# Optimization experiments

Hardware: AMD Instinct MI355X
Metric: run time of the kernel (lower is better)

Reference implementation:

```python
import jax, jax.numpy as jnp
import numpy as np

WS = 8          # window_size
SHIFT = 4       # shift_size
HEADS = 8
HD = 32         # head_dim
DIM = 256       # embedding_dim
PWS = 8         # pretrained_window_size
EPS = 1e-5


def _rel_tables():
    # log-spaced relative coords table, shape ((2*WS-1)^2, 2)
    r = np.arange(-(WS - 1), WS, dtype=np.float32)
    tb = np.stack(np.meshgrid(r, r, indexing='ij'), 0).reshape(2, -1).T
    tb = tb / (PWS - 1) * 8.0
    tb = np.sign(tb) * np.log2(np.abs(tb) + 1.0) / np.log2(8.0)
    # relative position index, shape (m, m)
    ch = np.arange(WS)
    coords = np.stack(np.meshgrid(ch, ch, indexing='ij'), 0).reshape(2, -1)
    rel = (coords[:, :, None] - coords[:, None, :]).transpose(1, 2, 0).astype(np.int64)
    rel[..., 0] += WS - 1
    rel[..., 1] += WS - 1
    rel[..., 0] *= 2 * WS - 1
    return tb.astype(np.float32), rel.sum(-1)


def _shift_mask(h, w):
    # standard Swin SW-MSA mask: region labels -> -100 where regions differ
    img = np.zeros((h, w), np.int32)
    cnt = 0
    for hs in (slice(0, h - WS), slice(h - WS, h - SHIFT), slice(h - SHIFT, h)):
        for wsl in (slice(0, w - WS), slice(w - WS, w - SHIFT), slice(w - SHIFT, w)):
            img[hs, wsl] = cnt
            cnt += 1
    nh, nw = h // WS, w // WS
    m = WS * WS
    mw = img.reshape(nh, WS, nw, WS).transpose(0, 2, 1, 3).reshape(nh * nw, m)
    return np.where(mw[:, None, :] != mw[:, :, None], -100.0, 0.0).astype(np.float32)


def _ln(x, g, b):
    mu = x.mean(-1, keepdims=True)
    var = ((x - mu) ** 2).mean(-1, keepdims=True)
    return (x - mu) * jax.lax.rsqrt(var + EPS) * g + b


def setup_inputs() -> dict:
    key = jax.random.key(0)
    ks = jax.random.split(key, 8)
    s = 0.02
    return {
        'x': jax.random.normal(ks[0], (2, DIM, 256, 256), jnp.float32),
        'qkv_w': jax.random.normal(ks[1], (DIM, 3 * HEADS * HD), jnp.float32) * s,
        'logit_scale': jnp.full((HEADS,), np.log(10.0), jnp.float32),
        'proj_w': jax.random.normal(ks[2], (HEADS * HD, DIM), jnp.float32) * s,
        'proj_b': jnp.zeros((DIM,), jnp.float32),
        'ln1_w': jnp.ones((DIM,), jnp.float32),
        'ln1_b': jnp.zeros((DIM,), jnp.float32),
        'fc1_w': jax.random.normal(ks[3], (DIM, 4 * DIM), jnp.float32) * s,
        'fc1_b': jnp.zeros((4 * DIM,), jnp.float32),
        'fc2_w': jax.random.normal(ks[4], (4 * DIM, DIM), jnp.float32) * s,
        'fc2_b': jnp.zeros((DIM,), jnp.float32),
        'ln2_w': jnp.ones((DIM,), jnp.float32),
        'ln2_b': jnp.zeros((DIM,), jnp.float32),
        'cpb_w1': jax.random.normal(ks[5], (2, 512), jnp.float32) * s,
        'cpb_b1': jnp.zeros((512,), jnp.float32),
        'cpb_w2': jax.random.normal(ks[6], (512, HEADS), jnp.float32) * s,
    }


def reference(x, qkv_w, logit_scale, proj_w, proj_b, ln1_w, ln1_b,
              fc1_w, fc1_b, fc2_w, fc2_b, ln2_w, ln2_b,
              cpb_w1, cpb_b1, cpb_w2):
    b, c, h, w = x.shape
    nh, nw = h // WS, w // WS
    Nw, m = nh * nw, WS * WS
    tb_np, idx_np = _rel_tables()
    smask = jnp.asarray(_shift_mask(h, w))              # (Nw, m, m)

    # cyclic shift
    xs = jnp.roll(x, (-SHIFT, -SHIFT), axis=(2, 3))

    # relative position bias via MLP, then 16*sigmoid
    bt = jax.nn.relu(jnp.asarray(tb_np) @ cpb_w1 + cpb_b1) @ cpb_w2   # (T, H)
    rpe = bt[jnp.asarray(idx_np).reshape(-1)].reshape(m, m, HEADS)
    bias = 16.0 * jax.nn.sigmoid(rpe.transpose(2, 0, 1))              # (H, m, m)
    amask = bias[None] + smask[:, None]                               # (Nw, H, m, m)

    # window partition: (b, c, h, w) -> (b, Nw, m, c)
    xw = xs.reshape(b, c, nh, WS, nw, WS).transpose(0, 2, 4, 3, 5, 1).reshape(b, Nw, m, c)

    # cosine attention
    qkv = (xw @ qkv_w).reshape(b, Nw, m, 3, HEADS, HD).transpose(3, 0, 1, 4, 2, 5)
    q, k, v = qkv[0], qkv[1], qkv[2]                                  # (b, Nw, H, m, HD)
    qn = q / jnp.maximum(jnp.linalg.norm(q, axis=-1, keepdims=True), 1e-12)
    kn = k / jnp.maximum(jnp.linalg.norm(k, axis=-1, keepdims=True), 1e-12)
    scale = jnp.exp(jnp.minimum(logit_scale, np.log(100.0)))          # (H,)
    logits = jnp.einsum('bnhid,bnhjd->bnhij', qn, kn) * scale[None, None, :, None, None]
    logits = logits + amask[None]
    p = jax.nn.softmax(logits, axis=-1)
    o = jnp.einsum('bnhij,bnhjd->bnhid', p, v)
    o = o.transpose(0, 1, 3, 2, 4).reshape(b, Nw, m, HEADS * HD) @ proj_w + proj_b

    # post-norm residuals
    y = _ln(o, ln1_w, ln1_b) + xw
    mlp = jax.nn.gelu(y @ fc1_w + fc1_b, approximate=False) @ fc2_w + fc2_b
    y = _ln(mlp, ln2_w, ln2_b) + y

    # window reverse + un-shift
    xr = y.reshape(b, nh, nw, WS, WS, c).transpose(0, 5, 1, 3, 2, 4).reshape(b, c, h, w)
    return jnp.roll(xr, (SHIFT, SHIFT), axis=(2, 3))
```

## Files before the change

### kernel.cpp

```cpp
#include <hip/hip_runtime.h>
#include <hip/hip_bf16.h>

typedef __attribute__((ext_vector_type(4))) float f32x4;
typedef __attribute__((ext_vector_type(8))) short s16x8;
typedef __attribute__((ext_vector_type(4))) unsigned short u16x4;

#define L_XW   0
#define L_SLAB 32768
#define L_NQ   131072
#define L_NK   133120
#define L_Y    131072
#define L_H0   0
#define L_H1   32768
#define L_H2   65536
#define L_H3   98304
#define L_MB   0
#define SMEM_BYTES 163840

#define WSO_BIAS   0
#define WSO_QKVW   131072
#define WSO_PROJW  524288
#define WSO_FC1W   655360
#define WSO_FC2W   1179648
#define WSO_SIN    1703936ULL
#define WSO_SOUT   68812800ULL

#define LOG2E 1.4426950408f

__device__ __forceinline__ unsigned short f2bf(float f) {
  __hip_bfloat16 h = __float2bfloat16(f);
  return __builtin_bit_cast(unsigned short, h);
}
__device__ __forceinline__ float bf2f(unsigned short b) {
  union { unsigned u; float f; } v; v.u = ((unsigned)b) << 16;
  return v.f;
}
__device__ __forceinline__ int swzb(int row, int byteoff) {
  return byteoff ^ ((row & 7) << 4);
}

__global__ __launch_bounds__(256)
void prep_kernel(const float* __restrict__ qkv_w,
                 const float* __restrict__ proj_w,
                 const float* __restrict__ fc1_w,
                 const float* __restrict__ fc2_w,
                 const float* __restrict__ cpb_w1,
                 const float* __restrict__ cpb_b1,
                 const float* __restrict__ cpb_w2,
                 const float* __restrict__ x,
                 const float* __restrict__ ls,
                 unsigned char* __restrict__ wsb) {
  __shared__ float tile[64][66];
  const int bid = blockIdx.x;
  const int tid = threadIdx.x;

  if (bid < 3072) {
    int e = bid * 256 + tid;
    const float* src; unsigned short* dst; int K, N; int eo; bool perm;
    if (e < 196608)       { eo = e;          src = qkv_w;  dst = (unsigned short*)(wsb + WSO_QKVW);  K = 256;  N = 768;  perm = false; }
    else if (e < 262144)  { eo = e - 196608; src = proj_w; dst = (unsigned short*)(wsb + WSO_PROJW); K = 256;  N = 256;  perm = true; }
    else if (e < 524288)  { eo = e - 262144; src = fc1_w;  dst = (unsigned short*)(wsb + WSO_FC1W);  K = 256;  N = 1024; perm = false; }
    else                  { eo = e - 524288; src = fc2_w;  dst = (unsigned short*)(wsb + WSO_FC2W);  K = 1024; N = 256;  perm = true; }
    int j = eo & 7, c = (eo >> 3) & 15, rest = eo >> 7;
    int Kg = K >> 3;
    int kg = rest % Kg, nt = rest / Kg;
    int s = kg * 8 + j;
    if (perm) s = (s & ~31) | ((s & 1) << 4) | ((s & 31) >> 1);
    dst[eo] = f2bf(src[s * N + nt * 16 + c]);
  } else if (bid == 3072) {
    float (*bt)[8] = (float(*)[8])&tile[0][0];
    for (int t = tid; t < 225; t += 256) {
      int a = t / 15, b = t % 15;
      float r0 = (float)(a - 7) * (8.0f / 7.0f);
      float r1 = (float)(b - 7) * (8.0f / 7.0f);
      float f0 = (r0 >= 0.f ? 1.f : -1.f) * log2f(fabsf(r0) + 1.f) * (1.f / 3.f);
      float f1 = (r1 >= 0.f ? 1.f : -1.f) * log2f(fabsf(r1) + 1.f) * (1.f / 3.f);
      float acc[8] = {0.f,0.f,0.f,0.f,0.f,0.f,0.f,0.f};
      for (int k = 0; k < 512; ++k) {
        float hv = f0 * cpb_w1[k] + f1 * cpb_w1[512 + k] + cpb_b1[k];
        hv = fmaxf(hv, 0.f);
        #pragma unroll
        for (int h = 0; h < 8; ++h) acc[h] += hv * cpb_w2[k * 8 + h];
      }
      #pragma unroll
      for (int h = 0; h < 8; ++h) bt[t][h] = acc[h];
    }
    __syncthreads();
    float* biasp = (float*)(wsb + WSO_BIAS);
    for (int e = tid; e < 32768; e += 256) {
      int nn = e & 3, cc = (e >> 2) & 15, i = (e >> 6) & 63, h = e >> 12;
      int j = nn * 16 + cc;
      int dr = (i >> 3) - (j >> 3) + 7, dc = (i & 7) - (j & 7) + 7;
      float v = bt[dr * 15 + dc][h];
      float scale = __expf(fminf(ls[h], 4.6051702f));
      biasp[e] = LOG2E * (16.f / (1.f + expf(-v)) - (scale + 16.f));
    }
  } else {
    int b2 = bid - 3073;
    int pb = b2 & 1023;
    int cg = (b2 >> 10) & 3;
    int b  = b2 >> 12;
    int p0 = pb * 64, c0 = cg * 64;
    unsigned short* sg = (unsigned short*)(wsb + WSO_SIN);

    int pi = tid & 63, cq = tid >> 6;
    for (int r = 0; r < 16; ++r) {
      int c = cq * 16 + r;
      tile[pi][c] = x[((size_t)(b * 256 + c0 + c)) * 65536 + p0 + pi];
    }
    __syncthreads();
    int po = tid >> 2, co = tid & 3;
    s16x8 pk0, pk1;
    #pragma unroll
    for (int j = 0; j < 8; ++j) {
      pk0[j] = (short)f2bf(tile[po][co * 16 + j]);
      pk1[j] = (short)f2bf(tile[po][co * 16 + 8 + j]);
    }
    unsigned short* dp = sg + ((size_t)b * 65536 + p0 + po) * 256 + c0 + co * 16;
    *(s16x8*)(dp) = pk0;
    *(s16x8*)(dp + 8) = pk1;
  }
}

__global__ __launch_bounds__(256)
void transpose_out_kernel(const unsigned char* __restrict__ wsb, float* __restrict__ out) {
  __shared__ float tile[64][65];
  int pb = blockIdx.x & 1023;
  int cg = (blockIdx.x >> 10) & 3;
  int b  = blockIdx.x >> 12;
  int p0 = pb * 64, c0 = cg * 64;
  int tid = threadIdx.x;
  const unsigned short* sg = (const unsigned short*)(wsb + WSO_SOUT);

  int pi = tid >> 2, cq = tid & 3;
  const unsigned short* rp = sg + ((size_t)b * 65536 + p0 + pi) * 256 + c0 + cq * 16;
  s16x8 a0 = *(const s16x8*)(rp);
  s16x8 a1 = *(const s16x8*)(rp + 8);
  #pragma unroll
  for (int j = 0; j < 8; ++j) {
    tile[pi][cq * 16 + j]     = bf2f((unsigned short)a0[j]);
    tile[pi][cq * 16 + 8 + j] = bf2f((unsigned short)a1[j]);
  }
  __syncthreads();
  int ci = tid >> 6, pi2 = tid & 63;
  for (int r = 0; r < 16; ++r) {
    int c = ci * 16 + r;
    out[((size_t)(b * 256 + c0 + c)) * 65536 + p0 + pi2] = tile[pi2][c];
  }
}

__global__ __launch_bounds__(512, 2)
void swin_block_kernel(const float* __restrict__ ls,
                       const float* __restrict__ proj_b,
                       const float* __restrict__ ln1w, const float* __restrict__ ln1b,
                       const float* __restrict__ fc1b,
                       const float* __restrict__ fc2b,
                       const float* __restrict__ ln2w, const float* __restrict__ ln2b,
                       unsigned char* __restrict__ wsb) {
  extern __shared__ char sm[];
  const int tid = threadIdx.x;
  const int w = tid >> 6;
  const int lane = tid & 63;
  const int g = lane >> 4;
  const int c16 = lane & 15;

  const int blk = blockIdx.x;
  const int bb = blk >> 10;
  const int widx = blk & 1023;
  const int wi = widx >> 5, wj = widx & 31;

  const f32x4* biasv = (const f32x4*)(wsb + WSO_BIAS);
  const unsigned short* qkvw = (const unsigned short*)(wsb + WSO_QKVW);
  const unsigned short* projw = (const unsigned short*)(wsb + WSO_PROJW);
  const unsigned short* fc1w = (const unsigned short*)(wsb + WSO_FC1W);
  const unsigned short* fc2w = (const unsigned short*)(wsb + WSO_FC2W);
  const unsigned short* sin_ = (const unsigned short*)(wsb + WSO_SIN);
  unsigned short* sout = (unsigned short*)(wsb + WSO_SOUT);

  #pragma unroll
  for (int it = 0; it < 4; ++it) {
    int u = tid + it * 512;
    int t = u >> 5, cu = u & 31;
    int rp = (wi * 8 + (t >> 3) + 4) & 255;
    int cp = (wj * 8 + (t & 7) + 4) & 255;
    size_t pix = (size_t)bb * 65536 + rp * 256 + cp;
    s16x8 v = *(const s16x8*)(sin_ + pix * 256 + cu * 8);
    *(s16x8*)(sm + L_XW + t * 512 + swzb(t, cu * 16)) = v;
  }
  __syncthreads();

  char* const QB = sm + L_SLAB + w * 12288;

  {
    int tiles[6] = {2*w, 2*w+1, 16+2*w, 17+2*w, 32+2*w, 33+2*w};
    f32x4 acc[6][4];
    #pragma unroll
    for (int a = 0; a < 6; ++a)
      #pragma unroll
      for (int b = 0; b < 4; ++b) acc[a][b] = f32x4{0.f,0.f,0.f,0.f};
    __builtin_amdgcn_s_setprio(1);
    #pragma unroll 4
    for (int k0 = 0; k0 < 256; k0 += 32) {
      s16x8 af[4];
      #pragma unroll
      for (int mt = 0; mt < 4; ++mt) {
        int row = mt * 16 + c16;
        af[mt] = *(const s16x8*)(sm + L_XW + row * 512 + swzb(row, (k0 + g * 8) * 2));
      }
      #pragma unroll
      for (int ct = 0; ct < 6; ++ct) {
        s16x8 bfr = *(const s16x8*)(qkvw + ((tiles[ct] * 32 + (k0 >> 3) + g) * 16 + c16) * 8);
        #pragma unroll
        for (int mt = 0; mt < 4; ++mt)
          acc[ct][mt] = __builtin_amdgcn_mfma_f32_16x16x32_bf16(af[mt], bfr, acc[ct][mt], 0, 0, 0);
      }
    }
    __builtin_amdgcn_s_setprio(0);
    #pragma unroll
    for (int mt = 0; mt < 4; ++mt)
      #pragma unroll
      for (int r = 0; r < 4; ++r) {
        int i = mt * 16 + 4 * g + r;
        unsigned uq = (unsigned)f2bf(acc[0][mt][r]) | ((unsigned)f2bf(acc[1][mt][r]) << 16);
        unsigned uk = (unsigned)f2bf(acc[2][mt][r]) | ((unsigned)f2bf(acc[3][mt][r]) << 16);
        *(unsigned*)(QB + i * 128 + swzb(i, c16 * 4)) = uq;
        *(unsigned*)(QB + i * 128 + swzb(i, 64 + c16 * 4)) = uk;
      }
    #pragma unroll
    for (int dt = 0; dt < 2; ++dt)
      #pragma unroll
      for (int r = 0; r < 4; ++r) {
        int d = dt * 16 + c16;
        u16x4 vv;
        #pragma unroll
        for (int mt = 0; mt < 4; ++mt) vv[mt] = f2bf(acc[4 + dt][mt][r]);
        *(u16x4*)(QB + 8192 + d * 128 + swzb(d, 8 * (4 * g + r))) = vv;
      }
  }
  {
    float lsc2 = LOG2E * __expf(fminf(ls[w], 4.6051702f));
    float sq = 0.f, sk2 = 0.f;
    #pragma unroll
    for (int cc4 = 0; cc4 < 4; ++cc4) {
      s16x8 qv = *(const s16x8*)(QB + lane * 128 + swzb(lane, cc4 * 16));
      s16x8 kv = *(const s16x8*)(QB + lane * 128 + swzb(lane, 64 + cc4 * 16));
      #pragma unroll
      for (int e = 0; e < 8; ++e) {
        float a = bf2f((unsigned short)qv[e]); sq  += a * a;
        float b = bf2f((unsigned short)kv[e]); sk2 += b * b;
      }
    }
    ((float*)(sm + L_NQ))[w * 64 + lane] = lsc2 * __builtin_amdgcn_rsqf(fmaxf(sq, 1e-24f));
    ((float*)(sm + L_NK))[w * 64 + lane] = __builtin_amdgcn_rsqf(fmaxf(sk2, 1e-24f));
  }

  {
    s16x8 qf[4];
    #pragma unroll
    for (int mt = 0; mt < 4; ++mt) {
      int row = mt * 16 + c16;
      qf[mt] = *(const s16x8*)(QB + row * 128 + swzb(row, g * 16));
    }
    f32x4 S[4][4];
    __builtin_amdgcn_s_setprio(1);
    #pragma unroll
    for (int nt = 0; nt < 4; ++nt) {
      int row = nt * 16 + c16;
      s16x8 kf = *(const s16x8*)(QB + row * 128 + swzb(row, 64 + g * 16));
      #pragma unroll
      for (int mt = 0; mt < 4; ++mt)
        S[mt][nt] = __builtin_amdgcn_mfma_f32_16x16x32_bf16(qf[mt], kf, f32x4{0.f,0.f,0.f,0.f}, 0, 0, 0);
    }
    __builtin_amdgcn_s_setprio(0);
    const float* nqp = (const float*)(sm + L_NQ) + w * 64;
    const float* nkp = (const float*)(sm + L_NK) + w * 64;
    float rk4[4];
    #pragma unroll
    for (int nt = 0; nt < 4; ++nt) rk4[nt] = nkp[nt * 16 + c16];

    const bool edge = (wi == 31) || (wj == 31);
    if (edge) {
      int labj[4];
      #pragma unroll
      for (int nt = 0; nt < 4; ++nt) {
        int jj = nt * 16 + c16;
        int tr = jj >> 3, tc = jj & 7;
        labj[nt] = ((wi == 31) ? (tr >= 4 ? 2 : 1) : 0) * 3 + ((wj == 31) ? (tc >= 4 ? 2 : 1) : 0);
      }
      #pragma unroll
      for (int mt = 0; mt < 4; ++mt)
        #pragma unroll
        for (int r = 0; r < 4; ++r) {
          int i = mt * 16 + 4 * g + r;
          float rq = nqp[i];
          f32x4 bb4 = biasv[(w * 64 + i) * 16 + c16];
          int tr = i >> 3, tc = i & 7;
          int labi = ((wi == 31) ? (tr >= 4 ? 2 : 1) : 0) * 3 + ((wj == 31) ? (tc >= 4 ? 2 : 1) : 0);
          u16x4 pk;
          #pragma unroll
          for (int nt = 0; nt < 4; ++nt) {
            float vx = fmaf(S[mt][nt][r] * rk4[nt], rq, bb4[nt]);
            if (labi != labj[nt]) vx -= 144.2695f;
            pk[nt] = f2bf(__builtin_amdgcn_exp2f(vx));
          }
          *(u16x4*)(QB + i * 128 + swzb(i, c16 * 8)) = pk;
        }
    } else {
      #pragma unroll
      for (int mt = 0; mt < 4; ++mt)
        #pragma unroll
        for (int r = 0; r < 4; ++r) {
          int i = mt * 16 + 4 * g + r;
          float rq = nqp[i];
          f32x4 bb4 = biasv[(w * 64 + i) * 16 + c16];
          u16x4 pk;
          #pragma unroll
          for (int nt = 0; nt < 4; ++nt) {
            float vx = fmaf(S[mt][nt][r] * rk4[nt], rq, bb4[nt]);
            pk[nt] = f2bf(__builtin_amdgcn_exp2f(vx));
          }
          *(u16x4*)(QB + i * 128 + swzb(i, c16 * 8)) = pk;
        }
    }

    s16x8 ones;
    #pragma unroll
    for (int e = 0; e < 8; ++e) ones[e] = (short)0x3F80;
    f32x4 O[4][2], RS[4];
    #pragma unroll
    for (int a = 0; a < 4; ++a) {
      O[a][0] = f32x4{0.f,0.f,0.f,0.f};
      O[a][1] = f32x4{0.f,0.f,0.f,0.f};
      RS[a]   = f32x4{0.f,0.f,0.f,0.f};
    }
    __builtin_amdgcn_s_setprio(1);
    #pragma unroll
    for (int k0 = 0; k0 < 64; k0 += 32) {
      s16x8 pf[4];
      #pragma unroll
      for (int mt = 0; mt < 4; ++mt) {
        int row = mt * 16 + c16;
        pf[mt] = *(const s16x8*)(QB + row * 128 + swzb(row, (k0 + g * 8) * 2));
      }
      #pragma unroll
      for (int nt = 0; nt < 2; ++nt) {
        int d = nt * 16 + c16;
        s16x8 vf = *(const s16x8*)(QB + 8192 + d * 128 + swzb(d, (k0 + g * 8) * 2));
        #pragma unroll
        for (int mt = 0; mt < 4; ++mt)
          O[mt][nt] = __builtin_amdgcn_mfma_f32_16x16x32_bf16(pf[mt], vf, O[mt][nt], 0, 0, 0);
      }
      #pragma unroll
      for (int mt = 0; mt < 4; ++mt)
        RS[mt] = __builtin_amdgcn_mfma_f32_16x16x32_bf16(pf[mt], ones, RS[mt], 0, 0, 0);
    }
    __builtin_amdgcn_s_setprio(0);
    #pragma unroll
    for (int mt = 0; mt < 4; ++mt)
      #pragma unroll
      for (int r = 0; r < 4; ++r) {
        float inv = __builtin_amdgcn_rcpf(fmaxf(RS[mt][r], 1e-35f));
        int i = mt * 16 + 4 * g + r;
        unsigned u = (unsigned)f2bf(O[mt][0][r] * inv) | ((unsigned)f2bf(O[mt][1][r] * inv) << 16);
        *(unsigned*)(QB + i * 128 + swzb(i, c16 * 4)) = u;
      }
  }
  __syncthreads();

  {
    f32x4 aP[2][4];
    #pragma unroll
    for (int a = 0; a < 2; ++a)
      #pragma unroll
      for (int b = 0; b < 4; ++b) aP[a][b] = f32x4{0.f,0.f,0.f,0.f};
    __builtin_amdgcn_s_setprio(1);
    #pragma unroll 2
    for (int k0 = 0; k0 < 256; k0 += 32) {
      int hk = k0 >> 5;
      const char* OBk = sm + L_SLAB + hk * 12288;
      s16x8 af[4];
      #pragma unroll
      for (int mt = 0; mt < 4; ++mt) {
        int row = mt * 16 + c16;
        af[mt] = *(const s16x8*)(OBk + row * 128 + swzb(row, g * 16));
      }
      #pragma unroll
      for (int t2 = 0; t2 < 2; ++t2) {
        s16x8 bfr = *(const s16x8*)(projw + (((2*w + t2) * 32 + 4*hk + g) * 16 + c16) * 8);
        #pragma unroll
        for (int mt = 0; mt < 4; ++mt)
          aP[t2][mt] = __builtin_amdgcn_mfma_f32_16x16x32_bf16(af[mt], bfr, aP[t2][mt], 0, 0, 0);
      }
    }
    __builtin_amdgcn_s_setprio(0);
    #pragma unroll
    for (int t2 = 0; t2 < 2; ++t2) {
      int col = (2*w + t2) * 16 + c16;
      float pb = proj_b[col];
      #pragma unroll
      for (int mt = 0; mt < 4; ++mt)
        #pragma unroll
        for (int r = 0; r < 4; ++r) {
          int i = mt * 16 + 4 * g + r;
          *(unsigned short*)(sm + L_Y + i * 512 + swzb(i, col * 2)) = f2bf(aP[t2][mt][r] + pb);
        }
    }
  }
  __syncthreads();

  {
    int t = tid >> 3, oc = tid & 7;
    float v[32];
    float s1 = 0.f;
    #pragma unroll
    for (int b2 = 0; b2 < 4; ++b2) {
      s16x8 vb = *(const s16x8*)(sm + L_Y + t * 512 + swzb(t, oc * 64 + b2 * 16));
      #pragma unroll
      for (int e = 0; e < 8; ++e) { float fv = bf2f((unsigned short)vb[e]); v[b2*8+e] = fv; s1 += fv; }
    }
    s1 += __shfl_xor(s1, 1);
    s1 += __shfl_xor(s1, 2);
    s1 += __shfl_xor(s1, 4);
    float mu = s1 * (1.f / 256.f);
    float s2 = 0.f;
    #pragma unroll
    for (int e = 0; e < 32; ++e) { float d = v[e] - mu; s2 += d * d; }
    s2 += __shfl_xor(s2, 1);
    s2 += __shfl_xor(s2, 2);
    s2 += __shfl_xor(s2, 4);
    float rs = __builtin_amdgcn_rsqf(s2 * (1.f / 256.f) + 1e-5f);
    #pragma unroll
    for (int b2 = 0; b2 < 4; ++b2) {
      s16x8 xb = *(const s16x8*)(sm + L_XW + t * 512 + swzb(t, oc * 64 + b2 * 16));
      s16x8 yb;
      #pragma unroll
      for (int e = 0; e < 8; ++e) {
        int c = oc * 32 + b2 * 8 + e;
        float yv = (v[b2*8+e] - mu) * rs * ln1w[c] + ln1b[c] + bf2f((unsigned short)xb[e]);
        yb[e] = (short)f2bf(yv);
      }
      *(s16x8*)(sm + L_Y + t * 512 + swzb(t, oc * 64 + b2 * 16)) = yb;
    }
  }
  __syncthreads();

  {
    const int Hoff[4] = {L_H0, L_H1, L_H2, L_H3};
    #pragma unroll 1
    for (int cp = 0; cp < 2; ++cp) {
      f32x4 acc1[2][2][4];
      #pragma unroll
      for (int a = 0; a < 2; ++a)
        #pragma unroll
        for (int b = 0; b < 2; ++b)
          #pragma unroll
          for (int m = 0; m < 4; ++m) acc1[a][b][m] = f32x4{0.f,0.f,0.f,0.f};
      __builtin_amdgcn_s_setprio(1);
      for (int k0 = 0; k0 < 256; k0 += 32) {
        s16x8 af[4];
        #pragma unroll
        for (int mt = 0; mt < 4; ++mt) {
          int row = mt * 16 + c16;
          af[mt] = *(const s16x8*)(sm + L_Y + row * 512 + swzb(row, (k0 + g * 8) * 2));
        }
        #pragma unroll
        for (int cc2 = 0; cc2 < 2; ++cc2) {
          int cc = cp * 2 + cc2;
          #pragma unroll
          for (int t2 = 0; t2 < 2; ++t2) {
            int gt = cc * 16 + 2*w + t2;
            s16x8 bfr = *(const s16x8*)(fc1w + ((gt * 32 + (k0 >> 3) + g) * 16 + c16) * 8);
            #pragma unroll
            for (int mt = 0; mt < 4; ++mt)
              acc1[cc2][t2][mt] = __builtin_amdgcn_mfma_f32_16x16x32_bf16(af[mt], bfr, acc1[cc2][t2][mt], 0, 0, 0);
          }
        }
      }
      __builtin_amdgcn_s_setprio(0);
      #pragma unroll
      for (int cc2 = 0; cc2 < 2; ++cc2) {
        int cc = cp * 2 + cc2;
        char* HB = sm + Hoff[cc];
        float b1v0 = fc1b[cc * 256 + 32 * w + c16];
        float b1v1 = fc1b[cc * 256 + 32 * w + 16 + c16];
        #pragma unroll
        for (int mt = 0; mt < 4; ++mt)
          #pragma unroll
          for (int r = 0; r < 4; ++r) {
            int i = mt * 16 + 4 * g + r;
            float u0 = acc1[cc2][0][mt][r] + b1v0;
            float u1 = acc1[cc2][1][mt][r] + b1v1;
            float e0 = __builtin_amdgcn_exp2f(-2.45538f * u0);
            float e1 = __builtin_amdgcn_exp2f(-2.45538f * u1);
            float g0 = u0 * __builtin_amdgcn_rcpf(1.f + e0);
            float g1 = u1 * __builtin_amdgcn_rcpf(1.f + e1);
            unsigned u = (unsigned)f2bf(g0) | ((unsigned)f2bf(g1) << 16);
            *(unsigned*)(HB + i * 512 + swzb(i, w * 64 + c16 * 4)) = u;
          }
      }
    }
  }
  __syncthreads();

  f32x4 acc2[2][4];
  #pragma unroll
  for (int a = 0; a < 2; ++a)
    #pragma unroll
    for (int b = 0; b < 4; ++b) acc2[a][b] = f32x4{0.f,0.f,0.f,0.f};
  {
    const int Hoff[4] = {L_H0, L_H1, L_H2, L_H3};
    __builtin_amdgcn_s_setprio(1);
    #pragma unroll 1
    for (int cc = 0; cc < 4; ++cc) {
      const char* HB = sm + Hoff[cc];
      for (int k0 = 0; k0 < 256; k0 += 32) {
        s16x8 af[4];
        #pragma unroll
        for (int mt = 0; mt < 4; ++mt) {
          int row = mt * 16 + c16;
          af[mt] = *(const s16x8*)(HB + row * 512 + swzb(row, (k0 + g * 8) * 2));
        }
        #pragma unroll
        for (int t2 = 0; t2 < 2; ++t2) {
          int kg = cc * 32 + (k0 >> 3) + g;
          s16x8 bfr = *(const s16x8*)(fc2w + (((2*w + t2) * 128 + kg) * 16 + c16) * 8);
          #pragma unroll
          for (int mt = 0; mt < 4; ++mt)
            acc2[t2][mt] = __builtin_amdgcn_mfma_f32_16x16x32_bf16(af[mt], bfr, acc2[t2][mt], 0, 0, 0);
        }
      }
    }
    __builtin_amdgcn_s_setprio(0);
  }
  __syncthreads();

  #pragma unroll
  for (int t2 = 0; t2 < 2; ++t2) {
    int col = (2*w + t2) * 16 + c16;
    float b2v = fc2b[col];
    #pragma unroll
    for (int mt = 0; mt < 4; ++mt)
      #pragma unroll
      for (int r = 0; r < 4; ++r) {
        int i = mt * 16 + 4 * g + r;
        *(unsigned short*)(sm + L_MB + i * 512 + swzb(i, col * 2)) = f2bf(acc2[t2][mt][r] + b2v);
      }
  }
  __syncthreads();

  {
    int t2 = tid >> 3, oc = tid & 7;
    float v[32];
    float s1 = 0.f;
    #pragma unroll
    for (int b2 = 0; b2 < 4; ++b2) {
      s16x8 vb = *(const s16x8*)(sm + L_MB + t2 * 512 + swzb(t2, oc * 64 + b2 * 16));
      #pragma unroll
      for (int e = 0; e < 8; ++e) { float fv = bf2f((unsigned short)vb[e]); v[b2*8+e] = fv; s1 += fv; }
    }
    s1 += __shfl_xor(s1, 1);
    s1 += __shfl_xor(s1, 2);
    s1 += __shfl_xor(s1, 4);
    float mu = s1 * (1.f / 256.f);
    float s2 = 0.f;
    #pragma unroll
    for (int e = 0; e < 32; ++e) { float d = v[e] - mu; s2 += d * d; }
    s2 += __shfl_xor(s2, 1);
    s2 += __shfl_xor(s2, 2);
    s2 += __shfl_xor(s2, 4);
    float rs = __builtin_amdgcn_rsqf(s2 * (1.f / 256.f) + 1e-5f);
    int rp = (wi * 8 + (t2 >> 3) + 4) & 255;
    int cp = (wj * 8 + (t2 & 7) + 4) & 255;
    size_t pix = (size_t)bb * 65536 + rp * 256 + cp;
    unsigned short* so = sout + pix * 256 + oc * 32;
    #pragma unroll
    for (int b2 = 0; b2 < 4; ++b2) {
      s16x8 yb = *(const s16x8*)(sm + L_Y + t2 * 512 + swzb(t2, oc * 64 + b2 * 16));
      s16x8 pk;
      #pragma unroll
      for (int e = 0; e < 8; ++e) {
        int c = oc * 32 + b2 * 8 + e;
        float yv = (v[b2*8+e] - mu) * rs * ln2w[c] + ln2b[c] + bf2f((unsigned short)yb[e]);
        pk[e] = (short)f2bf(yv);
      }
      *(s16x8*)(so + b2 * 8) = pk;
    }
  }
}

extern "C" void kernel_launch(void* const* d_in, const int* in_sizes, int n_in,
                              void* d_out, int out_size, void* d_ws, size_t ws_size,
                              hipStream_t stream) {
  const float* x      = (const float*)d_in[0];
  const float* qkv_w  = (const float*)d_in[1];
  const float* ls     = (const float*)d_in[2];
  const float* proj_w = (const float*)d_in[3];
  const float* proj_b = (const float*)d_in[4];
  const float* ln1w   = (const float*)d_in[5];
  const float* ln1b   = (const float*)d_in[6];
  const float* fc1_w  = (const float*)d_in[7];
  const float* fc1b   = (const float*)d_in[8];
  const float* fc2_w  = (const float*)d_in[9];
  const float* fc2b   = (const float*)d_in[10];
  const float* ln2w   = (const float*)d_in[11];
  const float* ln2b   = (const float*)d_in[12];
  const float* cpb_w1 = (const float*)d_in[13];
  const float* cpb_b1 = (const float*)d_in[14];
  const float* cpb_w2 = (const float*)d_in[15];
  unsigned char* wsb = (unsigned char*)d_ws;
  float* out = (float*)d_out;

  hipFuncSetAttribute(reinterpret_cast<const void*>(swin_block_kernel),
                      hipFuncAttributeMaxDynamicSharedMemorySize, SMEM_BYTES);

  prep_kernel<<<11265, 256, 0, stream>>>(qkv_w, proj_w, fc1_w, fc2_w,
                                         cpb_w1, cpb_b1, cpb_w2, x, ls, wsb);
  swin_block_kernel<<<2048, 512, SMEM_BYTES, stream>>>(
      ls, proj_b, ln1w, ln1b, fc1b, fc2b, ln2w, ln2b, wsb);
  transpose_out_kernel<<<8192, 256, 0, stream>>>(wsb, out);
}
```

Before: 468.2 us.

## Halve block to 4 waves, loop heads in two passes, fuse MLP chunks

New measurement: 1.077 ms. 130% more time.

```diff
diff --git a/kernel.cpp b/kernel.cpp
--- a/kernel.cpp
+++ b/kernel.cpp
@@ -7,15 +7,10 @@
 
 #define L_XW   0
 #define L_SLAB 32768
-#define L_NQ   131072
-#define L_NK   133120
-#define L_Y    131072
-#define L_H0   0
-#define L_H1   32768
-#define L_H2   65536
-#define L_H3   98304
+#define L_Y    32768
+#define L_H    0
 #define L_MB   0
-#define SMEM_BYTES 163840
+#define SMEM_BYTES 81920
 
 #define WSO_BIAS   0
 #define WSO_QKVW   131072
@@ -149,7 +144,7 @@
   }
 }
 
-__global__ __launch_bounds__(512, 2)
+__global__ __launch_bounds__(256, 2)
 void swin_block_kernel(const float* __restrict__ ls,
                        const float* __restrict__ proj_b,
                        const float* __restrict__ ln1w, const float* __restrict__ ln1b,
@@ -159,7 +154,7 @@
                        unsigned char* __restrict__ wsb) {
   extern __shared__ char sm[];
   const int tid = threadIdx.x;
-  const int w = tid >> 6;
+  const int ws = tid >> 6;
   const int lane = tid & 63;
   const int g = lane >> 4;
   const int c16 = lane & 15;
@@ -178,8 +173,8 @@
   unsigned short* sout = (unsigned short*)(wsb + WSO_SOUT);
 
   #pragma unroll
-  for (int it = 0; it < 4; ++it) {
-    int u = tid + it * 512;
+  for (int it = 0; it < 8; ++it) {
+    int u = tid + it * 256;
     int t = u >> 5, cu = u & 31;
     int rp = (wi * 8 + (t >> 3) + 4) & 255;
     int cp = (wj * 8 + (t & 7) + 4) & 255;
@@ -189,194 +184,179 @@
   }
   __syncthreads();
 
-  char* const QB = sm + L_SLAB + w * 12288;
-
-  {
-    int tiles[6] = {2*w, 2*w+1, 16+2*w, 17+2*w, 32+2*w, 33+2*w};
-    f32x4 acc[6][4];
-    #pragma unroll
-    for (int a = 0; a < 6; ++a)
-      #pragma unroll
-      for (int b = 0; b < 4; ++b) acc[a][b] = f32x4{0.f,0.f,0.f,0.f};
-    __builtin_amdgcn_s_setprio(1);
-    #pragma unroll 4
-    for (int k0 = 0; k0 < 256; k0 += 32) {
-      s16x8 af[4];
+  char* const QB = sm + L_SLAB + ws * 12288;
+
+  f32x4 accP[4][4];
+  #pragma unroll
+  for (int a = 0; a < 4; ++a)
+    #pragma unroll
+    for (int b = 0; b < 4; ++b) accP[a][b] = f32x4{0.f,0.f,0.f,0.f};
+
+  #pragma unroll 1
+  for (int b = 0; b < 2; ++b) {
+    const int hb = b * 4 + ws;
+    {
+      int tiles[6] = {2*hb, 2*hb+1, 16+2*hb, 17+2*hb, 32+2*hb, 33+2*hb};
+      f32x4 acc[6][4];
+      #pragma unroll
+      for (int a = 0; a < 6; ++a)
+        #pragma unroll
+        for (int m = 0; m < 4; ++m) acc[a][m] = f32x4{0.f,0.f,0.f,0.f};
+      __builtin_amdgcn_s_setprio(1);
+      #pragma unroll 2
+      for (int k0 = 0; k0 < 256; k0 += 32) {
+        s16x8 af[4];
+        #pragma unroll
+        for (int mt = 0; mt < 4; ++mt) {
+          int row = mt * 16 + c16;
+          af[mt] = *(const s16x8*)(sm + L_XW + row * 512 + swzb(row, (k0 + g * 8) * 2));
+        }
+        #pragma unroll
+        for (int ct = 0; ct < 6; ++ct) {
+          s16x8 bfr = *(const s16x8*)(qkvw + ((tiles[ct] * 32 + (k0 >> 3) + g) * 16 + c16) * 8);
+          #pragma unroll
+          for (int mt = 0; mt < 4; ++mt)
+            acc[ct][mt] = __builtin_amdgcn_mfma_f32_16x16x32_bf16(af[mt], bfr, acc[ct][mt], 0, 0, 0);
+        }
+      }
+      __builtin_amdgcn_s_setprio(0);
+      float lsc2 = LOG2E * __expf(fminf(ls[hb], 4.6051702f));
+      #pragma unroll
+      for (int mt = 0; mt < 4; ++mt)
+        #pragma unroll
+        for (int r = 0; r < 4; ++r) {
+          int i = mt * 16 + 4 * g + r;
+          float q0 = acc[0][mt][r], q1 = acc[1][mt][r];
+          float k0v = acc[2][mt][r], k1v = acc[3][mt][r];
+          float sq = q0 * q0 + q1 * q1;
+          float sk = k0v * k0v + k1v * k1v;
+          sq += __shfl_xor(sq, 1); sq += __shfl_xor(sq, 2);
+          sq += __shfl_xor(sq, 4); sq += __shfl_xor(sq, 8);
+          sk += __shfl_xor(sk, 1); sk += __shfl_xor(sk, 2);
+          sk += __shfl_xor(sk, 4); sk += __shfl_xor(sk, 8);
+          float rq = lsc2 * __builtin_amdgcn_rsqf(fmaxf(sq, 1e-24f));
+          float rk = __builtin_amdgcn_rsqf(fmaxf(sk, 1e-24f));
+          unsigned uq = (unsigned)f2bf(q0 * rq) | ((unsigned)f2bf(q1 * rq) << 16);
+          unsigned uk = (unsigned)f2bf(k0v * rk) | ((unsigned)f2bf(k1v * rk) << 16);
+          *(unsigned*)(QB + i * 128 + swzb(i, c16 * 4)) = uq;
+          *(unsigned*)(QB + i * 128 + swzb(i, 64 + c16 * 4)) = uk;
+        }
+      #pragma unroll
+      for (int dt = 0; dt < 2; ++dt)
+        #pragma unroll
+        for (int r = 0; r < 4; ++r) {
+          int d = dt * 16 + c16;
+          u16x4 vv;
+          #pragma unroll
+          for (int mt = 0; mt < 4; ++mt) vv[mt] = f2bf(acc[4 + dt][mt][r]);
+          *(u16x4*)(QB + 8192 + d * 128 + swzb(d, 8 * (4 * g + r))) = vv;
+        }
+    }
+    {
+      s16x8 qf[4];
       #pragma unroll
       for (int mt = 0; mt < 4; ++mt) {
         int row = mt * 16 + c16;
-        af[mt] = *(const s16x8*)(sm + L_XW + row * 512 + swzb(row, (k0 + g * 8) * 2));
-      }
-      #pragma unroll
-      for (int ct = 0; ct < 6; ++ct) {
-        s16x8 bfr = *(const s16x8*)(qkvw + ((tiles[ct] * 32 + (k0 >> 3) + g) * 16 + c16) * 8);
-        #pragma unroll
-        for (int mt = 0; mt < 4; ++mt)
-          acc[ct][mt] = __builtin_amdgcn_mfma_f32_16x16x32_bf16(af[mt], bfr, acc[ct][mt], 0, 0, 0);
-      }
-    }
-    __builtin_amdgcn_s_setprio(0);
-    #pragma unroll
-    for (int mt = 0; mt < 4; ++mt)
-      #pragma unroll
-      for (int r = 0; r < 4; ++r) {
-        int i = mt * 16 + 4 * g + r;
-        unsigned uq = (unsigned)f2bf(acc[0][mt][r]) | ((unsigned)f2bf(acc[1][mt][r]) << 16);
-        unsigned uk = (unsigned)f2bf(acc[2][mt][r]) | ((unsigned)f2bf(acc[3][mt][r]) << 16);
-        *(unsigned*)(QB + i * 128 + swzb(i, c16 * 4)) = uq;
-        *(unsigned*)(QB + i * 128 + swzb(i, 64 + c16 * 4)) = uk;
-      }
-    #pragma unroll
-    for (int dt = 0; dt < 2; ++dt)
-      #pragma unroll
-      for (int r = 0; r < 4; ++r) {
-        int d = dt * 16 + c16;
-        u16x4 vv;
-        #pragma unroll
-        for (int mt = 0; mt < 4; ++mt) vv[mt] = f2bf(acc[4 + dt][mt][r]);
-        *(u16x4*)(QB + 8192 + d * 128 + swzb(d, 8 * (4 * g + r))) = vv;
-      }
-  }
-  {
-    float lsc2 = LOG2E * __expf(fminf(ls[w], 4.6051702f));
-    float sq = 0.f, sk2 = 0.f;
-    #pragma unroll
-    for (int cc4 = 0; cc4 < 4; ++cc4) {
-      s16x8 qv = *(const s16x8*)(QB + lane * 128 + swzb(lane, cc4 * 16));
-      s16x8 kv = *(const s16x8*)(QB + lane * 128 + swzb(lane, 64 + cc4 * 16));
-      #pragma unroll
-      for (int e = 0; e < 8; ++e) {
-        float a = bf2f((unsigned short)qv[e]); sq  += a * a;
-        float b = bf2f((unsigned short)kv[e]); sk2 += b * b;
-      }
-    }
-    ((float*)(sm + L_NQ))[w * 64 + lane] = lsc2 * __builtin_amdgcn_rsqf(fmaxf(sq, 1e-24f));
-    ((float*)(sm + L_NK))[w * 64 + lane] = __builtin_amdgcn_rsqf(fmaxf(sk2, 1e-24f));
-  }
-
-  {
-    s16x8 qf[4];
-    #pragma unroll
-    for (int mt = 0; mt < 4; ++mt) {
-      int row = mt * 16 + c16;
-      qf[mt] = *(const s16x8*)(QB + row * 128 + swzb(row, g * 16));
-    }
-    f32x4 S[4][4];
+        qf[mt] = *(const s16x8*)(QB + row * 128 + swzb(row, g * 16));
+      }
+      f32x4 S[4][4];
+      __builtin_amdgcn_s_setprio(1);
+      #pragma unroll
+      for (int nt = 0; nt < 4; ++nt) {
+        int row = nt * 16 + c16;
+        s16x8 kf = *(const s16x8*)(QB + row * 128 + swzb(row, 64 + g * 16));
+        #pragma unroll
+        for (int mt = 0; mt < 4; ++mt)
+          S[mt][nt] = __builtin_amdgcn_mfma_f32_16x16x32_bf16(qf[mt], kf, f32x4{0.f,0.f,0.f,0.f}, 0, 0, 0);
+      }
+      __builtin_amdgcn_s_setprio(0);
+      const bool edge = (wi == 31) || (wj == 31);
+      if (edge) {
+        int labj[4];
+        #pragma unroll
+        for (int nt = 0; nt < 4; ++nt) {
+          int jj = nt * 16 + c16;
+          int tr = jj >> 3, tc = jj & 7;
+          labj[nt] = ((wi == 31) ? (tr >= 4 ? 2 : 1) : 0) * 3 + ((wj == 31) ? (tc >= 4 ? 2 : 1) : 0);
+        }
+        #pragma unroll
+        for (int mt = 0; mt < 4; ++mt)
+          #pragma unroll
+          for (int r = 0; r < 4; ++r) {
+            int i = mt * 16 + 4 * g + r;
+            f32x4 bb4 = biasv[(hb * 64 + i) * 16 + c16];
+            int tr = i >> 3, tc = i & 7;
+            int labi = ((wi == 31) ? (tr >= 4 ? 2 : 1) : 0) * 3 + ((wj == 31) ? (tc >= 4 ? 2 : 1) : 0);
+            u16x4 pk;
+            #pragma unroll
+            for (int nt = 0; nt < 4; ++nt) {
+              float vx = S[mt][nt][r] + bb4[nt];
+              if (labi != labj[nt]) vx -= 144.2695f;
+              pk[nt] = f2bf(__builtin_amdgcn_exp2f(vx));
+            }
+            *(u16x4*)(QB + i * 128 + swzb(i, c16 * 8)) = pk;
+          }
+      } else {
+        #pragma unroll
+        for (int mt = 0; mt < 4; ++mt)
+          #pragma unroll
+          for (int r = 0; r < 4; ++r) {
+            int i = mt * 16 + 4 * g + r;
+            f32x4 bb4 = biasv[(hb * 64 + i) * 16 + c16];
+            u16x4 pk;
+            #pragma unroll
+            for (int nt = 0; nt < 4; ++nt)
+              pk[nt] = f2bf(__builtin_amdgcn_exp2f(S[mt][nt][r] + bb4[nt]));
+            *(u16x4*)(QB + i * 128 + swzb(i, c16 * 8)) = pk;
+          }
+      }
+      s16x8 ones;
+      #pragma unroll
+      for (int e = 0; e < 8; ++e) ones[e] = (short)0x3F80;
+      f32x4 O[4][2], RS[4];
+      #pragma unroll
+      for (int a = 0; a < 4; ++a) {
+        O[a][0] = f32x4{0.f,0.f,0.f,0.f};
+        O[a][1] = f32x4{0.f,0.f,0.f,0.f};
+        RS[a]   = f32x4{0.f,0.f,0.f,0.f};
+      }
+      __builtin_amdgcn_s_setprio(1);
+      #pragma unroll
+      for (int k0 = 0; k0 < 64; k0 += 32) {
+        s16x8 pf[4];
+        #pragma unroll
+        for (int mt = 0; mt < 4; ++mt) {
+          int row = mt * 16 + c16;
+          pf[mt] = *(const s16x8*)(QB + row * 128 + swzb(row, (k0 + g * 8) * 2));
+        }
+        #pragma unroll
+        for (int nt = 0; nt < 2; ++nt) {
+          int d = nt * 16 + c16;
+          s16x8 vf = *(const s16x8*)(QB + 8192 + d * 128 + swzb(d, (k0 + g * 8) * 2));
+          #pragma unroll
+          for (int mt = 0; mt < 4; ++mt)
+            O[mt][nt] = __builtin_amdgcn_mfma_f32_16x16x32_bf16(pf[mt], vf, O[mt][nt], 0, 0, 0);
+        }
+        #pragma unroll
+        for (int mt = 0; mt < 4; ++mt)
+          RS[mt] = __builtin_amdgcn_mfma_f32_16x16x32_bf16(pf[mt], ones, RS[mt], 0, 0, 0);
+      }
+      __builtin_amdgcn_s_setprio(0);
+      #pragma unroll
+      for (int mt = 0; mt < 4; ++mt)
+        #pragma unroll
+        for (int r = 0; r < 4; ++r) {
+          float inv = __builtin_amdgcn_rcpf(fmaxf(RS[mt][r], 1e-35f));
+          int i = mt * 16 + 4 * g + r;
+          unsigned u = (unsigned)f2bf(O[mt][0][r] * inv) | ((unsigned)f2bf(O[mt][1][r] * inv) << 16);
+          *(unsigned*)(QB + i * 128 + swzb(i, c16 * 4)) = u;
+        }
+    }
+    __syncthreads();
+
     __builtin_amdgcn_s_setprio(1);
-    #pragma unroll
-    for (int nt = 0; nt < 4; ++nt) {
-      int row = nt * 16 + c16;
-      s16x8 kf = *(const s16x8*)(QB + row * 128 + swzb(row, 64 + g * 16));
-      #pragma unroll
-      for (int mt = 0; mt < 4; ++mt)
-        S[mt][nt] = __builtin_amdgcn_mfma_f32_16x16x32_bf16(qf[mt], kf, f32x4{0.f,0.f,0.f,0.f}, 0, 0, 0);
-    }
-    __builtin_amdgcn_s_setprio(0);
-    const float* nqp = (const float*)(sm + L_NQ) + w * 64;
-    const float* nkp = (const float*)(sm + L_NK) + w * 64;
-    float rk4[4];
-    #pragma unroll
-    for (int nt = 0; nt < 4; ++nt) rk4[nt] = nkp[nt * 16 + c16];
-
-    const bool edge = (wi == 31) || (wj == 31);
-    if (edge) {
-      int labj[4];
-      #pragma unroll
-      for (int nt = 0; nt < 4; ++nt) {
-        int jj = nt * 16 + c16;
-        int tr = jj >> 3, tc = jj & 7;
-        labj[nt] = ((wi == 31) ? (tr >= 4 ? 2 : 1) : 0) * 3 + ((wj == 31) ? (tc >= 4 ? 2 : 1) : 0);
-      }
-      #pragma unroll
-      for (int mt = 0; mt < 4; ++mt)
-        #pragma unroll
-        for (int r = 0; r < 4; ++r) {
-          int i = mt * 16 + 4 * g + r;
-          float rq = nqp[i];
-          f32x4 bb4 = biasv[(w * 64 + i) * 16 + c16];
-          int tr = i >> 3, tc = i & 7;
-          int labi = ((wi == 31) ? (tr >= 4 ? 2 : 1) : 0) * 3 + ((wj == 31) ? (tc >= 4 ? 2 : 1) : 0);
-          u16x4 pk;
-          #pragma unroll
-          for (int nt = 0; nt < 4; ++nt) {
-            float vx = fmaf(S[mt][nt][r] * rk4[nt], rq, bb4[nt]);
-            if (labi != labj[nt]) vx -= 144.2695f;
-            pk[nt] = f2bf(__builtin_amdgcn_exp2f(vx));
-          }
-          *(u16x4*)(QB + i * 128 + swzb(i, c16 * 8)) = pk;
-        }
-    } else {
-      #pragma unroll
-      for (int mt = 0; mt < 4; ++mt)
-        #pragma unroll
-        for (int r = 0; r < 4; ++r) {
-          int i = mt * 16 + 4 * g + r;
-          float rq = nqp[i];
-          f32x4 bb4 = biasv[(w * 64 + i) * 16 + c16];
-          u16x4 pk;
-          #pragma unroll
-          for (int nt = 0; nt < 4; ++nt) {
-            float vx = fmaf(S[mt][nt][r] * rk4[nt], rq, bb4[nt]);
-            pk[nt] = f2bf(__builtin_amdgcn_exp2f(vx));
-          }
-          *(u16x4*)(QB + i * 128 + swzb(i, c16 * 8)) = pk;
-        }
-    }
-
-    s16x8 ones;
-    #pragma unroll
-    for (int e = 0; e < 8; ++e) ones[e] = (short)0x3F80;
-    f32x4 O[4][2], RS[4];
-    #pragma unroll
-    for (int a = 0; a < 4; ++a) {
-      O[a][0] = f32x4{0.f,0.f,0.f,0.f};
-      O[a][1] = f32x4{0.f,0.f,0.f,0.f};
-      RS[a]   = f32x4{0.f,0.f,0.f,0.f};
-    }
-    __builtin_amdgcn_s_setprio(1);
-    #pragma unroll
-    for (int k0 = 0; k0 < 64; k0 += 32) {
-      s16x8 pf[4];
-      #pragma unroll
-      for (int mt = 0; mt < 4; ++mt) {
-        int row = mt * 16 + c16;
-        pf[mt] = *(const s16x8*)(QB + row * 128 + swzb(row, (k0 + g * 8) * 2));
-      }
-      #pragma unroll
-      for (int nt = 0; nt < 2; ++nt) {
-        int d = nt * 16 + c16;
-        s16x8 vf = *(const s16x8*)(QB + 8192 + d * 128 + swzb(d, (k0 + g * 8) * 2));
-        #pragma unroll
-        for (int mt = 0; mt < 4; ++mt)
-          O[mt][nt] = __builtin_amdgcn_mfma_f32_16x16x32_bf16(pf[mt], vf, O[mt][nt], 0, 0, 0);
-      }
-      #pragma unroll
-      for (int mt = 0; mt < 4; ++mt)
-        RS[mt] = __builtin_amdgcn_mfma_f32_16x16x32_bf16(pf[mt], ones, RS[mt], 0, 0, 0);
-    }
-    __builtin_amdgcn_s_setprio(0);
-    #pragma unroll
-    for (int mt = 0; mt < 4; ++mt)
-      #pragma unroll
-      for (int r = 0; r < 4; ++r) {
-        float inv = __builtin_amdgcn_rcpf(fmaxf(RS[mt][r], 1e-35f));
-        int i = mt * 16 + 4 * g + r;
-        unsigned u = (unsigned)f2bf(O[mt][0][r] * inv) | ((unsigned)f2bf(O[mt][1][r] * inv) << 16);
-        *(unsigned*)(QB + i * 128 + swzb(i, c16 * 4)) = u;
-      }
-  }
-  __syncthreads();
-
-  {
-    f32x4 aP[2][4];
-    #pragma unroll
-    for (int a = 0; a < 2; ++a)
-      #pragma unroll
-      for (int b = 0; b < 4; ++b) aP[a][b] = f32x4{0.f,0.f,0.f,0.f};
-    __builtin_amdgcn_s_setprio(1);
-    #pragma unroll 2
-    for (int k0 = 0; k0 < 256; k0 += 32) {
-      int hk = k0 >> 5;
+    #pragma unroll 1
+    for (int hk = 0; hk < 4; ++hk) {
       const char* OBk = sm + L_SLAB + hk * 12288;
       s16x8 af[4];
       #pragma unroll
@@ -385,158 +365,143 @@
         af[mt] = *(const s16x8*)(OBk + row * 128 + swzb(row, g * 16));
       }
       #pragma unroll
-      for (int t2 = 0; t2 < 2; ++t2) {
-        s16x8 bfr = *(const s16x8*)(projw + (((2*w + t2) * 32 + 4*hk + g) * 16 + c16) * 8);
-        #pragma unroll
-        for (int mt = 0; mt < 4; ++mt)
-          aP[t2][mt] = __builtin_amdgcn_mfma_f32_16x16x32_bf16(af[mt], bfr, aP[t2][mt], 0, 0, 0);
+      for (int t2 = 0; t2 < 4; ++t2) {
+        s16x8 bfr = *(const s16x8*)(projw + (((4*ws + t2) * 32 + (b * 4 + hk) * 4 + g) * 16 + c16) * 8);
+        #pragma unroll
+        for (int mt = 0; mt < 4; ++mt)
+          accP[t2][mt] = __builtin_amdgcn_mfma_f32_16x16x32_bf16(af[mt], bfr, accP[t2][mt], 0, 0, 0);
       }
     }
     __builtin_amdgcn_s_setprio(0);
-    #pragma unroll
-    for (int t2 = 0; t2 < 2; ++t2) {
-      int col = (2*w + t2) * 16 + c16;
-      float pb = proj_b[col];
-      #pragma unroll
-      for (int mt = 0; mt < 4; ++mt)
-        #pragma unroll
-        for (int r = 0; r < 4; ++r) {
-          int i = mt * 16 + 4 * g + r;
-          *(unsigned short*)(sm + L_Y + i * 512 + swzb(i, col * 2)) = f2bf(aP[t2][mt][r] + pb);
-        }
-    }
+    __syncthreads();
+  }
+
+  #pragma unroll
+  for (int t2 = 0; t2 < 4; ++t2) {
+    int col = (4*ws + t2) * 16 + c16;
+    float pb = proj_b[col];
+    #pragma unroll
+    for (int mt = 0; mt < 4; ++mt)
+      #pragma unroll
+      for (int r = 0; r < 4; ++r) {
+        int i = mt * 16 + 4 * g + r;
+        *(unsigned short*)(sm + L_Y + i * 512 + swzb(i, col * 2)) = f2bf(accP[t2][mt][r] + pb);
+      }
   }
   __syncthreads();
 
   {
-    int t = tid >> 3, oc = tid & 7;
-    float v[32];
+    int t = tid >> 2, oc = tid & 3;
+    float v[64];
     float s1 = 0.f;
     #pragma unroll
-    for (int b2 = 0; b2 < 4; ++b2) {
-      s16x8 vb = *(const s16x8*)(sm + L_Y + t * 512 + swzb(t, oc * 64 + b2 * 16));
+    for (int b2 = 0; b2 < 8; ++b2) {
+      s16x8 vb = *(const s16x8*)(sm + L_Y + t * 512 + swzb(t, oc * 128 + b2 * 16));
       #pragma unroll
       for (int e = 0; e < 8; ++e) { float fv = bf2f((unsigned short)vb[e]); v[b2*8+e] = fv; s1 += fv; }
     }
     s1 += __shfl_xor(s1, 1);
     s1 += __shfl_xor(s1, 2);
-    s1 += __shfl_xor(s1, 4);
     float mu = s1 * (1.f / 256.f);
     float s2 = 0.f;
     #pragma unroll
-    for (int e = 0; e < 32; ++e) { float d = v[e] - mu; s2 += d * d; }
+    for (int e = 0; e < 64; ++e) { float d = v[e] - mu; s2 += d * d; }
     s2 += __shfl_xor(s2, 1);
     s2 += __shfl_xor(s2, 2);
-    s2 += __shfl_xor(s2, 4);
     float rs = __builtin_amdgcn_rsqf(s2 * (1.f / 256.f) + 1e-5f);
     #pragma unroll
-    for (int b2 = 0; b2 < 4; ++b2) {
-      s16x8 xb = *(const s16x8*)(sm + L_XW + t * 512 + swzb(t, oc * 64 + b2 * 16));
+    for (int b2 = 0; b2 < 8; ++b2) {
+      s16x8 xb = *(const s16x8*)(sm + L_XW + t * 512 + swzb(t, oc * 128 + b2 * 16));
       s16x8 yb;
       #pragma unroll
       for (int e = 0; e < 8; ++e) {
-        int c = oc * 32 + b2 * 8 + e;
+        int c = oc * 64 + b2 * 8 + e;
         float yv = (v[b2*8+e] - mu) * rs * ln1w[c] + ln1b[c] + bf2f((unsigned short)xb[e]);
         yb[e] = (short)f2bf(yv);
       }
-      *(s16x8*)(sm + L_Y + t * 512 + swzb(t, oc * 64 + b2 * 16)) = yb;
+      *(s16x8*)(sm + L_Y + t * 512 + swzb(t, oc * 128 + b2 * 16)) = yb;
     }
   }
   __syncthreads();
 
-  {
-    const int Hoff[4] = {L_H0, L_H1, L_H2, L_H3};
-    #pragma unroll 1
-    for (int cp = 0; cp < 2; ++cp) {
-      f32x4 acc1[2][2][4];
-      #pragma unroll
-      for (int a = 0; a < 2; ++a)
-        #pragma unroll
-        for (int b = 0; b < 2; ++b)
-          #pragma unroll
-          for (int m = 0; m < 4; ++m) acc1[a][b][m] = f32x4{0.f,0.f,0.f,0.f};
-      __builtin_amdgcn_s_setprio(1);
-      for (int k0 = 0; k0 < 256; k0 += 32) {
-        s16x8 af[4];
-        #pragma unroll
-        for (int mt = 0; mt < 4; ++mt) {
-          int row = mt * 16 + c16;
-          af[mt] = *(const s16x8*)(sm + L_Y + row * 512 + swzb(row, (k0 + g * 8) * 2));
-        }
-        #pragma unroll
-        for (int cc2 = 0; cc2 < 2; ++cc2) {
-          int cc = cp * 2 + cc2;
-          #pragma unroll
-          for (int t2 = 0; t2 < 2; ++t2) {
-            int gt = cc * 16 + 2*w + t2;
-            s16x8 bfr = *(const s16x8*)(fc1w + ((gt * 32 + (k0 >> 3) + g) * 16 + c16) * 8);
-            #pragma unroll
-            for (int mt = 0; mt < 4; ++mt)
-              acc1[cc2][t2][mt] = __builtin_amdgcn_mfma_f32_16x16x32_bf16(af[mt], bfr, acc1[cc2][t2][mt], 0, 0, 0);
-          }
-        }
-      }
-      __builtin_amdgcn_s_setprio(0);
-      #pragma unroll
-      for (int cc2 = 0; cc2 < 2; ++cc2) {
-        int cc = cp * 2 + cc2;
-        char* HB = sm + Hoff[cc];
-        float b1v0 = fc1b[cc * 256 + 32 * w + c16];
-        float b1v1 = fc1b[cc * 256 + 32 * w + 16 + c16];
+  f32x4 acc2[4][4];
+  #pragma unroll
+  for (int a = 0; a < 4; ++a)
+    #pragma unroll
+    for (int m = 0; m < 4; ++m) acc2[a][m] = f32x4{0.f,0.f,0.f,0.f};
+
+  #pragma unroll 1
+  for (int cc = 0; cc < 4; ++cc) {
+    f32x4 acc1[4][4];
+    #pragma unroll
+    for (int a = 0; a < 4; ++a)
+      #pragma unroll
+      for (int m = 0; m < 4; ++m) acc1[a][m] = f32x4{0.f,0.f,0.f,0.f};
+    __builtin_amdgcn_s_setprio(1);
+    for (int k0 = 0; k0 < 256; k0 += 32) {
+      s16x8 af[4];
+      #pragma unroll
+      for (int mt = 0; mt < 4; ++mt) {
+        int row = mt * 16 + c16;
+        af[mt] = *(const s16x8*)(sm + L_Y + row * 512 + swzb(row, (k0 + g * 8) * 2));
+      }
+      #pragma unroll
+      for (int ct = 0; ct < 4; ++ct) {
+        int gt = cc * 16 + ws * 4 + ct;
+        s16x8 bfr = *(const s16x8*)(fc1w + ((gt * 32 + (k0 >> 3) + g) * 16 + c16) * 8);
+        #pragma unroll
+        for (int mt = 0; mt < 4; ++mt)
+          acc1[ct][mt] = __builtin_amdgcn_mfma_f32_16x16x32_bf16(af[mt], bfr, acc1[ct][mt], 0, 0, 0);
+      }
+    }
+    __builtin_amdgcn_s_setprio(0);
+    {
+      float b1v[4];
+      #pragma unroll
+      for (int ct = 0; ct < 4; ++ct) b1v[ct] = fc1b[(cc * 16 + ws * 4 + ct) * 16 + c16];
+      #pragma unroll
+      for (int cp2 = 0; cp2 < 2; ++cp2) {
         #pragma unroll
         for (int mt = 0; mt < 4; ++mt)
           #pragma unroll
           for (int r = 0; r < 4; ++r) {
             int i = mt * 16 + 4 * g + r;
-            float u0 = acc1[cc2][0][mt][r] + b1v0;
-            float u1 = acc1[cc2][1][mt][r] + b1v1;
+            float u0 = acc1[cp2 * 2][mt][r] + b1v[cp2 * 2];
+            float u1 = acc1[cp2 * 2 + 1][mt][r] + b1v[cp2 * 2 + 1];
             float e0 = __builtin_amdgcn_exp2f(-2.45538f * u0);
             float e1 = __builtin_amdgcn_exp2f(-2.45538f * u1);
             float g0 = u0 * __builtin_amdgcn_rcpf(1.f + e0);
             float g1 = u1 * __builtin_amdgcn_rcpf(1.f + e1);
             unsigned u = (unsigned)f2bf(g0) | ((unsigned)f2bf(g1) << 16);
-            *(unsigned*)(HB + i * 512 + swzb(i, w * 64 + c16 * 4)) = u;
+            *(unsigned*)(sm + L_H + i * 512 + swzb(i, (ws * 2 + cp2) * 64 + c16 * 4)) = u;
           }
       }
     }
-  }
-  __syncthreads();
-
-  f32x4 acc2[2][4];
+    __syncthreads();
+    __builtin_amdgcn_s_setprio(1);
+    for (int k0 = 0; k0 < 256; k0 += 32) {
+      s16x8 af[4];
+      #pragma unroll
+      for (int mt = 0; mt < 4; ++mt) {
+        int row = mt * 16 + c16;
+        af[mt] = *(const s16x8*)(sm + L_H + row * 512 + swzb(row, (k0 + g * 8) * 2));
+      }
+      #pragma unroll
+      for (int t2 = 0; t2 < 4; ++t2) {
+        int kg = cc * 32 + (k0 >> 3) + g;
+        s16x8 bfr = *(const s16x8*)(fc2w + (((4*ws + t2) * 128 + kg) * 16 + c16) * 8);
+        #pragma unroll
+        for (int mt = 0; mt < 4; ++mt)
+          acc2[t2][mt] = __builtin_amdgcn_mfma_f32_16x16x32_bf16(af[mt], bfr, acc2[t2][mt], 0, 0, 0);
+      }
+    }
+    __builtin_amdgcn_s_setprio(0);
+    __syncthreads();
+  }
+
   #pragma unroll
-  for (int a = 0; a < 2; ++a)
-    #pragma unroll
-    for (int b = 0; b < 4; ++b) acc2[a][b] = f32x4{0.f,0.f,0.f,0.f};
-  {
-    const int Hoff[4] = {L_H0, L_H1, L_H2, L_H3};
-    __builtin_amdgcn_s_setprio(1);
-    #pragma unroll 1
-    for (int cc = 0; cc < 4; ++cc) {
-      const char* HB = sm + Hoff[cc];
-      for (int k0 = 0; k0 < 256; k0 += 32) {
-        s16x8 af[4];
-        #pragma unroll
-        for (int mt = 0; mt < 4; ++mt) {
-          int row = mt * 16 + c16;
-          af[mt] = *(const s16x8*)(HB + row * 512 + swzb(row, (k0 + g * 8) * 2));
-        }
-        #pragma unroll
-        for (int t2 = 0; t2 < 2; ++t2) {
-          int kg = cc * 32 + (k0 >> 3) + g;
-          s16x8 bfr = *(const s16x8*)(fc2w + (((2*w + t2) * 128 + kg) * 16 + c16) * 8);
-          #pragma unroll
-          for (int mt = 0; mt < 4; ++mt)
-            acc2[t2][mt] = __builtin_amdgcn_mfma_f32_16x16x32_bf16(af[mt], bfr, acc2[t2][mt], 0, 0, 0);
-        }
-      }
-    }
-    __builtin_amdgcn_s_setprio(0);
-  }
-  __syncthreads();
-
-  #pragma unroll
-  for (int t2 = 0; t2 < 2; ++t2) {
-    int col = (2*w + t2) * 16 + c16;
+  for (int t2 = 0; t2 < 4; ++t2) {
+    int col = (4*ws + t2) * 16 + c16;
     float b2v = fc2b[col];
     #pragma unroll
     for (int mt = 0; mt < 4; ++mt)
@@ -549,37 +514,35 @@
   __syncthreads();
 
   {
-    int t2 = tid >> 3, oc = tid & 7;
-    float v[32];
+    int t2 = tid >> 2, oc = tid & 3;
+    float v[64];
     float s1 = 0.f;
     #pragma unroll
-    for (int b2 = 0; b2 < 4; ++b2) {
-      s16x8 vb = *(const s16x8*)(sm + L_MB + t2 * 512 + swzb(t2, oc * 64 + b2 * 16));
+    for (int b2 = 0; b2 < 8; ++b2) {
+      s16x8 vb = *(const s16x8*)(sm + L_MB + t2 * 512 + swzb(t2, oc * 128 + b2 * 16));
       #pragma unroll
       for (int e = 0; e < 8; ++e) { float fv = bf2f((unsigned short)vb[e]); v[b2*8+e] = fv; s1 += fv; }
     }
     s1 += __shfl_xor(s1, 1);
     s1 += __shfl_xor(s1, 2);
-    s1 += __shfl_xor(s1, 4);
     float mu = s1 * (1.f / 256.f);
     float s2 = 0.f;
     #pragma unroll
-    for (int e = 0; e < 32; ++e) { float d = v[e] - mu; s2 += d * d; }
+    for (int e = 0; e < 64; ++e) { float d = v[e] - mu; s2 += d * d; }
     s2 += __shfl_xor(s2, 1);
     s2 += __shfl_xor(s2, 2);
-    s2 += __shfl_xor(s2, 4);
     float rs = __builtin_amdgcn_rsqf(s2 * (1.f / 256.f) + 1e-5f);
     int rp = (wi * 8 + (t2 >> 3) + 4) & 255;
     int cp = (wj * 8 + (t2 & 7) + 4) & 255;
     size_t pix = (size_t)bb * 65536 + rp * 256 + cp;
-    unsigned short* so = sout + pix * 256 + oc * 32;
-    #pragma unroll
-    for (int b2 = 0; b2 < 4; ++b2) {
-      s16x8 yb = *(const s16x8*)(sm + L_Y + t2 * 512 + swzb(t2, oc * 64 + b2 * 16));
+    unsigned short* so = sout + pix * 256 + oc * 64;
+    #pragma unroll
+    for (int b2 = 0; b2 < 8; ++b2) {
+      s16x8 yb = *(const s16x8*)(sm + L_Y + t2 * 512 + swzb(t2, oc * 128 + b2 * 16));
       s16x8 pk;
       #pragma unroll
       for (int e = 0; e < 8; ++e) {
-        int c = oc * 32 + b2 * 8 + e;
+        int c = oc * 64 + b2 * 8 + e;
         float yv = (v[b2*8+e] - mu) * rs * ln2w[c] + ln2b[c] + bf2f((unsigned short)yb[e]);
         pk[e] = (short)f2bf(yv);
       }
@@ -615,7 +578,7 @@
 
   prep_kernel<<<11265, 256, 0, stream>>>(qkv_w, proj_w, fc1_w, fc2_w,
                                          cpb_w1, cpb_b1, cpb_w2, x, ls, wsb);
-  swin_block_kernel<<<2048, 512, SMEM_BYTES, stream>>>(
+  swin_block_kernel<<<2048, 256, SMEM_BYTES, stream>>>(
       ls, proj_b, ln1w, ln1b, fc1b, fc2b, ln2w, ln2b, wsb);
   transpose_out_kernel<<<8192, 256, 0, stream>>>(wsb, out);
 }
```
